# Optimization experiments

Measured on AMD Instinct MI355X. Metric: run time of the kernel, lower is better.

Reference implementation:

```python
import jax, jax.numpy as jnp
import numpy as np

IN_C, HID, LSTM_H, OUT_C = 128, 128, 128, 2
N_NODES, N_EDGES, N_GRAPHS = 100000, 1600000, 256


def gcn_conv(x, src, dst, W, b, n_nodes):
    # h = XW, then symmetric-normalized aggregation with self loops (PyG GCNConv defaults)
    h = x @ W  # [N, H]
    loop = jnp.arange(n_nodes)
    s = jnp.concatenate([src, loop])
    d = jnp.concatenate([dst, loop])
    deg = jax.ops.segment_sum(jnp.ones_like(d, dtype=h.dtype), d, num_segments=n_nodes)
    dinv = jnp.where(deg > 0, jax.lax.rsqrt(deg), 0.0)
    norm = dinv[s] * dinv[d]  # [E+N]
    out = jax.ops.segment_sum(norm[:, None] * h[s], d, num_segments=n_nodes)
    return out + b


def setup_inputs() -> dict:
    key = jax.random.key(0)
    ks = jax.random.split(key, 16)
    x = jax.random.normal(ks[0], (N_NODES, IN_C), dtype=jnp.float32)
    edge_index = jax.random.randint(ks[1], (2, N_EDGES), 0, N_NODES)
    batch = jnp.sort(jax.random.randint(ks[2], (N_NODES,), 0, N_GRAPHS))
    sc = lambda *shape: 1.0 / np.sqrt(shape[0])
    W0 = jax.random.normal(ks[3], (IN_C, HID), jnp.float32) * sc(IN_C)
    b0 = jnp.zeros((HID,), jnp.float32)
    W1 = jax.random.normal(ks[4], (HID, HID), jnp.float32) * sc(HID)
    b1 = jnp.zeros((HID,), jnp.float32)
    W2 = jax.random.normal(ks[5], (HID, HID), jnp.float32) * sc(HID)
    b2 = jnp.zeros((HID,), jnp.float32)
    W_ih = jax.random.normal(ks[6], (4 * LSTM_H, HID), jnp.float32) * sc(HID)
    W_hh = jax.random.normal(ks[7], (4 * LSTM_H, LSTM_H), jnp.float32) * sc(LSTM_H)
    b_ih = jnp.zeros((4 * LSTM_H,), jnp.float32)
    b_hh = jnp.zeros((4 * LSTM_H,), jnp.float32)
    W_fc = jax.random.normal(ks[8], (OUT_C, LSTM_H), jnp.float32) * sc(LSTM_H)
    b_fc = jnp.zeros((OUT_C,), jnp.float32)
    return dict(x=x, edge_index=edge_index, batch=batch, num_graphs=N_GRAPHS,
                W0=W0, b0=b0, W1=W1, b1=b1, W2=W2, b2=b2,
                W_ih=W_ih, W_hh=W_hh, b_ih=b_ih, b_hh=b_hh, W_fc=W_fc, b_fc=b_fc)


def reference(x, edge_index, batch, num_graphs, W0, b0, W1, b1, W2, b2,
              W_ih, W_hh, b_ih, b_hh, W_fc, b_fc):
    n_nodes = x.shape[0]
    src, dst = edge_index[0], edge_index[1]
    h = x
    for W, b in ((W0, b0), (W1, b1), (W2, b2)):
        h = jax.nn.relu(gcn_conv(h, src, dst, W, b, n_nodes))
    # dropout: identity in eval mode
    # global_mean_pool over batch ids
    sums = jax.ops.segment_sum(h, batch, num_segments=num_graphs)  # [G, HID]
    cnts = jax.ops.segment_sum(jnp.ones((n_nodes,), h.dtype), batch, num_segments=num_graphs)
    pooled = sums / jnp.maximum(cnts, 1.0)[:, None]
    # single-step LSTM from zero state: h0 = c0 = 0 => W_hh contributes 0
    g = pooled @ W_ih.T + b_ih + b_hh  # [G, 4H]
    i, f, gg, o = jnp.split(g, 4, axis=-1)  # PyTorch gate order i,f,g,o
    c = jax.nn.sigmoid(i) * jnp.tanh(gg)
    hn = jax.nn.sigmoid(o) * jnp.tanh(c)
    return hn @ W_fc.T + b_fc
```

## Files before the change

### kernel.cpp

```cpp
#include <hip/hip_runtime.h>
#include <math.h>
#include <stdint.h>

#define HID 128
#define SCAN_CHUNK 1024
#define NBUCK_MAX 512
#define EDGE_TILE 8192
#define GEMM_ROWS 128
#define XS_STRIDE 136

typedef short bf16x8 __attribute__((ext_vector_type(8)));
typedef float f32x4 __attribute__((ext_vector_type(4)));

__device__ __forceinline__ unsigned int f2bf(float f) {
    union { float f; uint32_t i; } u; u.f = f;
    uint32_t r = u.i + 0x7fffu + ((u.i >> 16) & 1u);
    return r >> 16;
}
__device__ __forceinline__ float bf2f_lo(uint32_t x) {
    union { uint32_t i; float f; } t; t.i = x << 16; return t.f;
}
__device__ __forceinline__ float bf2f_hi(uint32_t x) {
    union { uint32_t i; float f; } t; t.i = x & 0xffff0000u; return t.f;
}

__global__ __launch_bounds__(256) void scan_phase1(const int* __restrict__ cnt,
                                                   int* __restrict__ blockSums,
                                                   float* __restrict__ dinv, int nN) {
    __shared__ int sdata[256];
    const int t = threadIdx.x;
    const int idx = blockIdx.x * SCAN_CHUNK + t * 4;
    int v0 = 0, v1 = 0, v2 = 0, v3 = 0;
    if (idx + 3 < nN) {
        int4 v = *(const int4*)(cnt + idx);
        v0 = v.x; v1 = v.y; v2 = v.z; v3 = v.w;
        float4 dv;
        dv.x = rsqrtf((float)v0 + 1.0f);
        dv.y = rsqrtf((float)v1 + 1.0f);
        dv.z = rsqrtf((float)v2 + 1.0f);
        dv.w = rsqrtf((float)v3 + 1.0f);
        *(float4*)(dinv + idx) = dv;
    } else {
        if (idx     < nN) { v0 = cnt[idx];     dinv[idx]     = rsqrtf((float)v0 + 1.0f); }
        if (idx + 1 < nN) { v1 = cnt[idx + 1]; dinv[idx + 1] = rsqrtf((float)v1 + 1.0f); }
        if (idx + 2 < nN) { v2 = cnt[idx + 2]; dinv[idx + 2] = rsqrtf((float)v2 + 1.0f); }
        if (idx + 3 < nN) { v3 = cnt[idx + 3]; dinv[idx + 3] = rsqrtf((float)v3 + 1.0f); }
    }
    sdata[t] = v0 + v1 + v2 + v3;
    __syncthreads();
#pragma unroll
    for (int off = 128; off > 0; off >>= 1) {
        if (t < off) sdata[t] += sdata[t + off];
        __syncthreads();
    }
    if (t == 0) blockSums[blockIdx.x] = sdata[0];
}

__global__ __launch_bounds__(256) void scan_phase2(int* __restrict__ blockSums, int nB) {
    __shared__ int sd[256];
    const int t = threadIdx.x;
    sd[t] = (t < nB) ? blockSums[t] : 0;
    __syncthreads();
#pragma unroll
    for (int off = 1; off < 256; off <<= 1) {
        int v = sd[t];
        int add = (t >= off) ? sd[t - off] : 0;
        __syncthreads();
        sd[t] = v + add;
        __syncthreads();
    }
    if (t < nB) blockSums[t] = (t > 0) ? sd[t - 1] : 0;
}

__global__ __launch_bounds__(256) void scan_phase3(const int* __restrict__ cnt,
                                                   const int* __restrict__ blockOffsets,
                                                   int* __restrict__ rowptr, int nN, int nE) {
    __shared__ int sdata[256];
    const int t = threadIdx.x;
    const int idx = blockIdx.x * SCAN_CHUNK + t * 4;
    int v0 = 0, v1 = 0, v2 = 0, v3 = 0;
    if (idx + 3 < nN) {
        int4 v = *(const int4*)(cnt + idx);
        v0 = v.x; v1 = v.y; v2 = v.z; v3 = v.w;
    } else {
        if (idx     < nN) v0 = cnt[idx];
        if (idx + 1 < nN) v1 = cnt[idx + 1];
        if (idx + 2 < nN) v2 = cnt[idx + 2];
        if (idx + 3 < nN) v3 = cnt[idx + 3];
    }
    sdata[t] = v0 + v1 + v2 + v3;
    __syncthreads();
#pragma unroll
    for (int off = 1; off < 256; off <<= 1) {
        int v = sdata[t];
        int add = (t >= off) ? sdata[t - off] : 0;
        __syncthreads();
        sdata[t] = v + add;
        __syncthreads();
    }
    const int pre = blockOffsets[blockIdx.x] + ((t > 0) ? sdata[t - 1] : 0);
    if (idx + 3 < nN) {
        *(int4*)(rowptr + idx) = make_int4(pre, pre + v0, pre + v0 + v1, pre + v0 + v1 + v2);
    } else {
        if (idx     < nN) rowptr[idx]     = pre;
        if (idx + 1 < nN) rowptr[idx + 1] = pre + v0;
        if (idx + 2 < nN) rowptr[idx + 2] = pre + v0 + v1;
        if (idx + 3 < nN) rowptr[idx + 3] = pre + v0 + v1 + v2;
    }
    if (blockIdx.x == 0 && t == 0) rowptr[nN] = nE;
}

__global__ __launch_bounds__(256) void bucket_count(const int* __restrict__ dst,
                                                    int* __restrict__ bcnt, int nE, int nB) {
    __shared__ int h[NBUCK_MAX];
    for (int i = threadIdx.x; i < nB; i += 256) h[i] = 0;
    __syncthreads();
    const int base = blockIdx.x * EDGE_TILE;
    const int end = min(base + EDGE_TILE, nE);
    for (int e = base + threadIdx.x; e < end; e += 256)
        atomicAdd(&h[dst[e] >> 8], 1);
    __syncthreads();
    for (int i = threadIdx.x; i < nB; i += 256)
        if (h[i]) atomicAdd(&bcnt[i], h[i]);
}

__global__ __launch_bounds__(512) void bucket_scan(const int* __restrict__ bcnt,
                                                   int* __restrict__ boff,
                                                   int* __restrict__ bcur, int nB) {
    __shared__ int sd[512];
    const int t = threadIdx.x;
    sd[t] = (t < nB) ? bcnt[t] : 0;
    __syncthreads();
#pragma unroll
    for (int off = 1; off < 512; off <<= 1) {
        int v = sd[t];
        int add = (t >= off) ? sd[t - off] : 0;
        __syncthreads();
        sd[t] = v + add;
        __syncthreads();
    }
    if (t < nB) {
        int ex = (t > 0) ? sd[t - 1] : 0;
        boff[t] = ex;
        bcur[t] = ex;
    }
}

__global__ __launch_bounds__(256) void bucket_scatter(const int* __restrict__ src,
                                                      const int* __restrict__ dst,
                                                      int* __restrict__ bcur,
                                                      unsigned int* __restrict__ ebuf,
                                                      int nE, int nB) {
    __shared__ int h[NBUCK_MAX];
    __shared__ int basearr[NBUCK_MAX];
    const int base = blockIdx.x * EDGE_TILE;
    const int end = min(base + EDGE_TILE, nE);
    for (int i = threadIdx.x; i < nB; i += 256) h[i] = 0;
    __syncthreads();
    for (int e = base + threadIdx.x; e < end; e += 256)
        atomicAdd(&h[dst[e] >> 8], 1);
    __syncthreads();
    for (int i = threadIdx.x; i < nB; i += 256) {
        int c = h[i];
        basearr[i] = c ? atomicAdd(&bcur[i], c) : 0;
        h[i] = 0;
    }
    __syncthreads();
    for (int e = base + threadIdx.x; e < end; e += 256) {
        int d = dst[e];
        int b = d >> 8;
        int pos = basearr[b] + atomicAdd(&h[b], 1);
        ebuf[pos] = ((unsigned)src[e] << 8) | ((unsigned)d & 255u);
    }
}

__global__ __launch_bounds__(256) void node_count(const unsigned int* __restrict__ ebuf,
                                                  const int* __restrict__ boff,
                                                  int* __restrict__ cnt, int nE, int nB, int nN) {
    __shared__ int h[256];
    h[threadIdx.x] = 0;
    __syncthreads();
    const int b = blockIdx.x;
    const int e0 = boff[b];
    const int e1 = (b + 1 < nB) ? boff[b + 1] : nE;
    for (int e = e0 + threadIdx.x; e < e1; e += 256)
        atomicAdd(&h[ebuf[e] & 255u], 1);
    __syncthreads();
    const int v = b * 256 + threadIdx.x;
    if (v < nN) cnt[v] = h[threadIdx.x];
}

__global__ __launch_bounds__(256) void csr_from_buckets(const unsigned int* __restrict__ ebuf,
                                                        const int* __restrict__ boff,
                                                        const int* __restrict__ rowptr,
                                                        int* __restrict__ ssrc, int nE, int nB) {
    __shared__ int cur[256];
    const int b = blockIdx.x;
    const int e0 = boff[b];
    const int e1 = (b + 1 < nB) ? boff[b + 1] : nE;
    const int nodeBase = b * 256;
    cur[threadIdx.x] = 0;
    __syncthreads();
    for (int e = e0 + threadIdx.x; e < e1; e += 256) {
        unsigned int ed = ebuf[e];
        int li = (int)(ed & 255u);
        int pos = rowptr[nodeBase + li] + atomicAdd(&cur[li], 1);
        ssrc[pos] = (int)(ed >> 8);
    }
}

__global__ __launch_bounds__(256) void wt_kernel(const float* __restrict__ W0,
                                                 const float* __restrict__ W1,
                                                 const float* __restrict__ W2,
                                                 unsigned short* __restrict__ Wtb) {
    int i = blockIdx.x * 256 + threadIdx.x;
    if (i < 3 * HID * HID) {
        int w = i >> 14, r = i & 16383;
        int n = r >> 7, k = r & 127;
        const float* W = (w == 0) ? W0 : (w == 1) ? W1 : W2;
        Wtb[i] = (unsigned short)f2bf(W[k * HID + n]);
    }
}

__global__ __launch_bounds__(256) void gemm_mfma_f32in(const float* __restrict__ X,
                                                       const uint4* __restrict__ Wtb,
                                                       const float* __restrict__ dinv,
                                                       unsigned int* __restrict__ Pb32,
                                                       int nN) {
    __shared__ short Xs[GEMM_ROWS * XS_STRIDE];
    __shared__ short Ws[HID * XS_STRIDE];
    const int tid = threadIdx.x;
    const int rowBase = blockIdx.x * GEMM_ROWS;
#pragma unroll
    for (int it = 0; it < 16; ++it) {
        int f = it * 256 + tid;
        int row = f >> 5, c = f & 31;
        int grow = rowBase + row;
        float4 v = make_float4(0.f, 0.f, 0.f, 0.f);
        if (grow < nN) v = *(const float4*)(X + (size_t)grow * HID + c * 4);
        uint2 o;
        o.x = f2bf(v.x) | (f2bf(v.y) << 16);
        o.y = f2bf(v.z) | (f2bf(v.w) << 16);
        *(uint2*)(&Xs[row * XS_STRIDE + c * 4]) = o;
    }
#pragma unroll
    for (int it = 0; it < 8; ++it) {
        int f = it * 256 + tid;
        int n = f >> 4, c = f & 15;
        *(uint4*)(&Ws[n * XS_STRIDE + c * 8]) = Wtb[f];
    }
    __syncthreads();
    const int wave = tid >> 6, lane = tid & 63;
    const int quad = lane >> 4, l16 = lane & 15;
    f32x4 acc[2][8] = {};
    const int kq = quad * 8;
#pragma unroll
    for (int ks = 0; ks < 4; ++ks) {
        const int k0 = ks * 32 + kq;
        bf16x8 a0 = *(const bf16x8*)(&Xs[(wave * 32 + l16) * XS_STRIDE + k0]);
        bf16x8 a1 = *(const bf16x8*)(&Xs[(wave * 32 + 16 + l16) * XS_STRIDE + k0]);
#pragma unroll
        for (int nt = 0; nt < 8; ++nt) {
            bf16x8 b = *(const bf16x8*)(&Ws[(nt * 16 + l16) * XS_STRIDE + k0]);
            acc[0][nt] = __builtin_amdgcn_mfma_f32_16x16x32_bf16(a0, b, acc[0][nt], 0, 0, 0);
            acc[1][nt] = __builtin_amdgcn_mfma_f32_16x16x32_bf16(a1, b, acc[1][nt], 0, 0, 0);
        }
    }
#pragma unroll
    for (int mt = 0; mt < 2; ++mt) {
        const int gr0 = rowBase + wave * 32 + mt * 16 + quad * 4;
#pragma unroll
        for (int r = 0; r < 4; ++r) {
            const int gr = gr0 + r;
            const bool ok = gr < nN;
            const float d = ok ? dinv[gr] : 0.f;
#pragma unroll
            for (int nt = 0; nt < 8; ++nt) {
                float v = d * acc[mt][nt][r];
                float vo = __shfl_xor(v, 1, 64);
                if (ok && !(l16 & 1)) {
                    Pb32[(size_t)gr * 64 + nt * 8 + (l16 >> 1)] = f2bf(v) | (f2bf(vo) << 16);
                }
            }
        }
    }
}

__device__ __forceinline__ void acc_bf8(const uint4 q, float* a) {
    union { uint32_t i; float f; } t;
    t.i = q.x << 16;          a[0] += t.f;
    t.i = q.x & 0xffff0000u;  a[1] += t.f;
    t.i = q.y << 16;          a[2] += t.f;
    t.i = q.y & 0xffff0000u;  a[3] += t.f;
    t.i = q.z << 16;          a[4] += t.f;
    t.i = q.z & 0xffff0000u;  a[5] += t.f;
    t.i = q.w << 16;          a[6] += t.f;
    t.i = q.w & 0xffff0000u;  a[7] += t.f;
}

__global__ __launch_bounds__(256) void fused_agg_gemm(const uint4* __restrict__ Pb,
                                                      const int* __restrict__ rowptr,
                                                      const int* __restrict__ ssrc,
                                                      const float* __restrict__ dinv,
                                                      const float* __restrict__ bias,
                                                      const uint4* __restrict__ Wtb,
                                                      unsigned int* __restrict__ Pout32,
                                                      int nN) {
    __shared__ short Ws[HID * XS_STRIDE];
    __shared__ short Hs[16 * XS_STRIDE];
    const int tid = threadIdx.x;
#pragma unroll
    for (int it = 0; it < 8; ++it) {
        int f = it * 256 + tid;
        int n = f >> 4, c = f & 15;
        *(uint4*)(&Ws[n * XS_STRIDE + c * 8]) = Wtb[f];
    }
    const int lane16 = tid & 15;
    const int grp = tid >> 4;
    const int v = blockIdx.x * 16 + grp;
    const bool ok = v < nN;
    float a0[8], a1[8], a2[8], a3[8];
#pragma unroll
    for (int i = 0; i < 8; ++i) { a0[i] = 0.f; a1[i] = 0.f; a2[i] = 0.f; a3[i] = 0.f; }
    uint4 q = make_uint4(0u, 0u, 0u, 0u);
    if (ok) {
        acc_bf8(Pb[(size_t)v * 16 + lane16], a0);
        int e = rowptr[v];
        const int e1 = rowptr[v + 1];
        for (; e + 4 <= e1; e += 4) {
            const int u0 = ssrc[e + 0], u1 = ssrc[e + 1], u2 = ssrc[e + 2], u3 = ssrc[e + 3];
            uint4 q0 = Pb[(size_t)u0 * 16 + lane16];
            uint4 q1 = Pb[(size_t)u1 * 16 + lane16];
            uint4 q2 = Pb[(size_t)u2 * 16 + lane16];
            uint4 q3 = Pb[(size_t)u3 * 16 + lane16];
            acc_bf8(q0, a0); acc_bf8(q1, a1); acc_bf8(q2, a2); acc_bf8(q3, a3);
        }
        for (; e < e1; ++e) {
            uint4 qe = Pb[(size_t)ssrc[e] * 16 + lane16];
            acc_bf8(qe, a1);
        }
        const float dv = dinv[v];
        const float4 bb0 = ((const float4*)bias)[lane16 * 2];
        const float4 bb1 = ((const float4*)bias)[lane16 * 2 + 1];
        float4 o0, o1;
        o0.x = fmaxf(fmaf(dv, (a0[0] + a1[0]) + (a2[0] + a3[0]), bb0.x), 0.f);
        o0.y = fmaxf(fmaf(dv, (a0[1] + a1[1]) + (a2[1] + a3[1]), bb0.y), 0.f);
        o0.z = fmaxf(fmaf(dv, (a0[2] + a1[2]) + (a2[2] + a3[2]), bb0.z), 0.f);
        o0.w = fmaxf(fmaf(dv, (a0[3] + a1[3]) + (a2[3] + a3[3]), bb0.w), 0.f);
        o1.x = fmaxf(fmaf(dv, (a0[4] + a1[4]) + (a2[4] + a3[4]), bb1.x), 0.f);
        o1.y = fmaxf(fmaf(dv, (a0[5] + a1[5]) + (a2[5] + a3[5]), bb1.y), 0.f);
        o1.z = fmaxf(fmaf(dv, (a0[6] + a1[6]) + (a2[6] + a3[6]), bb1.z), 0.f);
        o1.w = fmaxf(fmaf(dv, (a0[7] + a1[7]) + (a2[7] + a3[7]), bb1.w), 0.f);
        q.x = f2bf(o0.x) | (f2bf(o0.y) << 16);
        q.y = f2bf(o0.z) | (f2bf(o0.w) << 16);
        q.z = f2bf(o1.x) | (f2bf(o1.y) << 16);
        q.w = f2bf(o1.z) | (f2bf(o1.w) << 16);
    }
    *(uint4*)(&Hs[grp * XS_STRIDE + lane16 * 8]) = q;
    __syncthreads();
    const int wave = tid >> 6, lane = tid & 63;
    const int quad = lane >> 4, l16 = lane & 15;
    f32x4 acc[2] = {};
#pragma unroll
    for (int ks = 0; ks < 4; ++ks) {
        const int k0 = ks * 32 + quad * 8;
        bf16x8 a = *(const bf16x8*)(&Hs[l16 * XS_STRIDE + k0]);
#pragma unroll
        for (int nt = 0; nt < 2; ++nt) {
            bf16x8 b = *(const bf16x8*)(&Ws[((wave * 2 + nt) * 16 + l16) * XS_STRIDE + k0]);
            acc[nt] = __builtin_amdgcn_mfma_f32_16x16x32_bf16(a, b, acc[nt], 0, 0, 0);
        }
    }
#pragma unroll
    for (int r = 0; r < 4; ++r) {
        const int gr = blockIdx.x * 16 + quad * 4 + r;
        const bool okr = gr < nN;
        const float d = okr ? dinv[gr] : 0.f;
#pragma unroll
        for (int nt = 0; nt < 2; ++nt) {
            float val = d * acc[nt][r];
            float vo = __shfl_xor(val, 1, 64);
            if (okr && !(l16 & 1)) {
                Pout32[(size_t)gr * 64 + (wave * 2 + nt) * 8 + (l16 >> 1)] =
                    f2bf(val) | (f2bf(vo) << 16);
            }
        }
    }
}

__global__ __launch_bounds__(256) void agg_kernel(const uint4* __restrict__ Pb,
                                                  const int* __restrict__ rowptr,
                                                  const int* __restrict__ ssrc,
                                                  const float* __restrict__ dinv,
                                                  const float* __restrict__ bias,
                                                  uint4* __restrict__ Xb_out, int nN) {
    const int lane = threadIdx.x & 15;
    const int grp = threadIdx.x >> 4;
    const int v = blockIdx.x * 16 + grp;
    if (v >= nN) return;
    float a0[8], a1[8], a2[8], a3[8];
#pragma unroll
    for (int i = 0; i < 8; ++i) { a0[i] = 0.f; a1[i] = 0.f; a2[i] = 0.f; a3[i] = 0.f; }
    acc_bf8(Pb[(size_t)v * 16 + lane], a0);
    int e = rowptr[v];
    const int e1 = rowptr[v + 1];
    for (; e + 4 <= e1; e += 4) {
        const int u0 = ssrc[e + 0], u1 = ssrc[e + 1], u2 = ssrc[e + 2], u3 = ssrc[e + 3];
        uint4 q0 = Pb[(size_t)u0 * 16 + lane];
        uint4 q1 = Pb[(size_t)u1 * 16 + lane];
        uint4 q2 = Pb[(size_t)u2 * 16 + lane];
        uint4 q3 = Pb[(size_t)u3 * 16 + lane];
        acc_bf8(q0, a0); acc_bf8(q1, a1); acc_bf8(q2, a2); acc_bf8(q3, a3);
    }
    for (; e < e1; ++e) {
        uint4 q = Pb[(size_t)ssrc[e] * 16 + lane];
        acc_bf8(q, a1);
    }
    const float dv = dinv[v];
    const float4 bb0 = ((const float4*)bias)[lane * 2];
    const float4 bb1 = ((const float4*)bias)[lane * 2 + 1];
    float4 o0, o1;
    o0.x = fmaxf(fmaf(dv, (a0[0] + a1[0]) + (a2[0] + a3[0]), bb0.x), 0.f);
    o0.y = fmaxf(fmaf(dv, (a0[1] + a1[1]) + (a2[1] + a3[1]), bb0.y), 0.f);
    o0.z = fmaxf(fmaf(dv, (a0[2] + a1[2]) + (a2[2] + a3[2]), bb0.z), 0.f);
    o0.w = fmaxf(fmaf(dv, (a0[3] + a1[3]) + (a2[3] + a3[3]), bb0.w), 0.f);
    o1.x = fmaxf(fmaf(dv, (a0[4] + a1[4]) + (a2[4] + a3[4]), bb1.x), 0.f);
    o1.y = fmaxf(fmaf(dv, (a0[5] + a1[5]) + (a2[5] + a3[5]), bb1.y), 0.f);
    o1.z = fmaxf(fmaf(dv, (a0[6] + a1[6]) + (a2[6] + a3[6]), bb1.z), 0.f);
    o1.w = fmaxf(fmaf(dv, (a0[7] + a1[7]) + (a2[7] + a3[7]), bb1.w), 0.f);
    uint4 q;
    q.x = f2bf(o0.x) | (f2bf(o0.y) << 16);
    q.y = f2bf(o0.z) | (f2bf(o0.w) << 16);
    q.z = f2bf(o1.x) | (f2bf(o1.y) << 16);
    q.w = f2bf(o1.z) | (f2bf(o1.w) << 16);
    Xb_out[(size_t)v * 16 + lane] = q;
}

__global__ __launch_bounds__(256) void pool_lstm(const unsigned int* __restrict__ Xb32,
                                                 const int* __restrict__ batch,
                                                 const float* __restrict__ W_ih,
                                                 const float* __restrict__ b_ih,
                                                 const float* __restrict__ b_hh,
                                                 const float* __restrict__ W_fc,
                                                 const float* __restrict__ b_fc,
                                                 float* __restrict__ out, int nN) {
    __shared__ float sred[4][HID];
    __shared__ float pv[HID];
    __shared__ float r0[4], r1[4];
    __shared__ int sbounds[2];
    const int g = blockIdx.x;
    const int tid = threadIdx.x;
    if (tid == 0) {
        int lo = 0, hi = nN;
        while (lo < hi) { int m = (lo + hi) >> 1; if (batch[m] < g) lo = m + 1; else hi = m; }
        sbounds[0] = lo;
        hi = nN;
        while (lo < hi) { int m = (lo + hi) >> 1; if (batch[m] < g + 1) lo = m + 1; else hi = m; }
        sbounds[1] = lo;
    }
    __syncthreads();
    const int s = sbounds[0], e = sbounds[1];
    const int c2 = tid & 63;
    const int st = tid >> 6;
    float acc0 = 0.f, acc1 = 0.f;
    int v = s + st;
    for (; v + 12 < e; v += 16) {
        unsigned int q0 = Xb32[(size_t)(v     ) * 64 + c2];
        unsigned int q1 = Xb32[(size_t)(v +  4) * 64 + c2];
        unsigned int q2 = Xb32[(size_t)(v +  8) * 64 + c2];
        unsigned int q3 = Xb32[(size_t)(v + 12) * 64 + c2];
        acc0 += (bf2f_lo(q0) + bf2f_lo(q1)) + (bf2f_lo(q2) + bf2f_lo(q3));
        acc1 += (bf2f_hi(q0) + bf2f_hi(q1)) + (bf2f_hi(q2) + bf2f_hi(q3));
    }
    for (; v < e; v += 4) {
        unsigned int q = Xb32[(size_t)v * 64 + c2];
        acc0 += bf2f_lo(q);
        acc1 += bf2f_hi(q);
    }
    sred[st][c2 * 2] = acc0;
    sred[st][c2 * 2 + 1] = acc1;
    __syncthreads();
    if (st == 0) {
        const float inv = 1.0f / (float)max(e - s, 1);
        pv[c2 * 2]     = ((sred[0][c2 * 2] + sred[1][c2 * 2]) +
                          (sred[2][c2 * 2] + sred[3][c2 * 2])) * inv;
        pv[c2 * 2 + 1] = ((sred[0][c2 * 2 + 1] + sred[1][c2 * 2 + 1]) +
                          (sred[2][c2 * 2 + 1] + sred[3][c2 * 2 + 1])) * inv;
    }
    __syncthreads();
    float p0 = 0.f, p1 = 0.f;
    if (tid < HID) {
        const int j = tid;
        float di = b_ih[j] + b_hh[j];
        float dg = b_ih[256 + j] + b_hh[256 + j];
        float dO = b_ih[384 + j] + b_hh[384 + j];
        const float4* pv4 = (const float4*)pv;
#pragma unroll 4
        for (int k4 = 0; k4 < 32; ++k4) {
            float4 p = pv4[k4];
            float4 wi = *(const float4*)(W_ih + (size_t)j * HID + k4 * 4);
            float4 wg = *(const float4*)(W_ih + (size_t)(256 + j) * HID + k4 * 4);
            float4 wo = *(const float4*)(W_ih + (size_t)(384 + j) * HID + k4 * 4);
            di += p.x * wi.x + p.y * wi.y + p.z * wi.z + p.w * wi.w;
            dg += p.x * wg.x + p.y * wg.y + p.z * wg.z + p.w * wg.w;
            dO += p.x * wo.x + p.y * wo.y + p.z * wo.z + p.w * wo.w;
        }
        const float si = 1.0f / (1.0f + expf(-di));
        const float so = 1.0f / (1.0f + expf(-dO));
        const float c = si * tanhf(dg);
        const float hn = so * tanhf(c);
        p0 = hn * W_fc[j];
        p1 = hn * W_fc[HID + j];
    }
#pragma unroll
    for (int off = 32; off > 0; off >>= 1) {
        p0 += __shfl_down(p0, off, 64);
        p1 += __shfl_down(p1, off, 64);
    }
    const int w = tid >> 6, l = tid & 63;
    if (l == 0) { r0[w] = p0; r1[w] = p1; }
    __syncthreads();
    if (tid == 0) {
        out[g * 2 + 0] = (r0[0] + r0[1]) + (r0[2] + r0[3]) + b_fc[0];
        out[g * 2 + 1] = (r1[0] + r1[1]) + (r1[2] + r1[3]) + b_fc[1];
    }
}

extern "C" void kernel_launch(void* const* d_in, const int* in_sizes, int n_in,
                              void* d_out, int out_size, void* d_ws, size_t ws_size,
                              hipStream_t stream) {
    const float* x      = (const float*)d_in[0];
    const int*   eidx   = (const int*)d_in[1];
    const int*   batch  = (const int*)d_in[2];
    const float* W0     = (const float*)d_in[4];
    const float* b0     = (const float*)d_in[5];
    const float* W1     = (const float*)d_in[6];
    const float* b1     = (const float*)d_in[7];
    const float* W2     = (const float*)d_in[8];
    const float* b2     = (const float*)d_in[9];
    const float* W_ih   = (const float*)d_in[10];
    const float* b_ih   = (const float*)d_in[12];
    const float* b_hh   = (const float*)d_in[13];
    const float* W_fc   = (const float*)d_in[14];
    const float* b_fc   = (const float*)d_in[15];
    float* out = (float*)d_out;

    const int nN = in_sizes[0] / HID;
    const int nE = in_sizes[1] / 2;
    const int nG = out_size / 2;
    const int* src = eidx;
    const int* dst = eidx + nE;
    const int rowsPad = (nN + GEMM_ROWS - 1) & ~(GEMM_ROWS - 1);

    size_t off = 0;
    auto alloc = [&](size_t bytes) -> void* {
        void* p = (char*)d_ws + off;
        off += (bytes + 255) & ~(size_t)255;
        return p;
    };
    uint4* Pb     = (uint4*)alloc((size_t)nN * 16 * sizeof(uint4));
    uint4* Pb2    = (uint4*)alloc((size_t)nN * 16 * sizeof(uint4));
    uint4* Xb     = (uint4*)alloc((size_t)nN * 16 * sizeof(uint4));
    float* dinv   = (float*)alloc((size_t)nN * sizeof(float));
    int*   cnt    = (int*)alloc((size_t)nN * sizeof(int));
    int*   rowptr = (int*)alloc((size_t)(nN + 1) * sizeof(int));
    int*   ssrc   = (int*)alloc((size_t)nE * sizeof(int));
    unsigned int* ebuf = (unsigned int*)alloc((size_t)nE * sizeof(unsigned int));
    int*   blockSums = (int*)alloc(1024 * sizeof(int));
    int*   bcnt   = (int*)alloc(NBUCK_MAX * sizeof(int));
    int*   boff   = (int*)alloc(NBUCK_MAX * sizeof(int));
    int*   bcur   = (int*)alloc(NBUCK_MAX * sizeof(int));
    unsigned short* Wtb = (unsigned short*)alloc(3 * HID * HID * sizeof(unsigned short));
    (void)ws_size;

    const int scanBlocks = (nN + SCAN_CHUNK - 1) / SCAN_CHUNK;
    const int nB = (nN + 255) >> 8;
    const int tileBlocks = (nE + EDGE_TILE - 1) / EDGE_TILE;

    hipMemsetAsync(bcnt, 0, NBUCK_MAX * sizeof(int), stream);
    bucket_count<<<tileBlocks, 256, 0, stream>>>(dst, bcnt, nE, nB);
    bucket_scan<<<1, 512, 0, stream>>>(bcnt, boff, bcur, nB);
    bucket_scatter<<<tileBlocks, 256, 0, stream>>>(src, dst, bcur, ebuf, nE, nB);

    node_count<<<nB, 256, 0, stream>>>(ebuf, boff, cnt, nE, nB, nN);
    scan_phase1<<<scanBlocks, 256, 0, stream>>>(cnt, blockSums, dinv, nN);
    scan_phase2<<<1, 256, 0, stream>>>(blockSums, scanBlocks);
    scan_phase3<<<scanBlocks, 256, 0, stream>>>(cnt, blockSums, rowptr, nN, nE);
    csr_from_buckets<<<nB, 256, 0, stream>>>(ebuf, boff, rowptr, ssrc, nE, nB);

    wt_kernel<<<(3 * HID * HID + 255) / 256, 256, 0, stream>>>(W0, W1, W2, Wtb);

    const int gemmBlocks = rowsPad / GEMM_ROWS;
    const int aggBlocks = (nN + 15) / 16;
    const uint4* Wt1 = (const uint4*)(Wtb + HID * HID);
    const uint4* Wt2 = (const uint4*)(Wtb + 2 * HID * HID);

    gemm_mfma_f32in<<<gemmBlocks, 256, 0, stream>>>(x, (const uint4*)Wtb, dinv,
                                                    (unsigned int*)Pb, nN);
    fused_agg_gemm<<<aggBlocks, 256, 0, stream>>>(Pb, rowptr, ssrc, dinv, b0, Wt1,
                                                  (unsigned int*)Pb2, nN);
    fused_agg_gemm<<<aggBlocks, 256, 0, stream>>>(Pb2, rowptr, ssrc, dinv, b1, Wt2,
                                                  (unsigned int*)Pb, nN);
    agg_kernel<<<aggBlocks, 256, 0, stream>>>(Pb, rowptr, ssrc, dinv, b2, Xb, nN);

    pool_lstm<<<nG, 256, 0, stream>>>((const unsigned int*)Xb, batch,
                                      W_ih, b_ih, b_hh, W_fc, b_fc, out, nN);
}
```

Measured before the change: 457.0 us.

## Build CSR in one cooperative kernel with global atomics and grid syncs

```diff
diff --git a/kernel.cpp b/kernel.cpp
--- a/kernel.cpp
+++ b/kernel.cpp
@@ -1,13 +1,12 @@
 #include <hip/hip_runtime.h>
+#include <hip/hip_cooperative_groups.h>
 #include <math.h>
 #include <stdint.h>
 
 #define HID 128
-#define SCAN_CHUNK 1024
-#define NBUCK_MAX 512
-#define EDGE_TILE 8192
 #define GEMM_ROWS 128
 #define XS_STRIDE 136
+#define NBLK 256
 
 typedef short bf16x8 __attribute__((ext_vector_type(8)));
 typedef float f32x4 __attribute__((ext_vector_type(4)));
@@ -24,201 +23,101 @@
     union { uint32_t i; float f; } t; t.i = x & 0xffff0000u; return t.f;
 }
 
-__global__ __launch_bounds__(256) void scan_phase1(const int* __restrict__ cnt,
-                                                   int* __restrict__ blockSums,
-                                                   float* __restrict__ dinv, int nN) {
-    __shared__ int sdata[256];
-    const int t = threadIdx.x;
-    const int idx = blockIdx.x * SCAN_CHUNK + t * 4;
-    int v0 = 0, v1 = 0, v2 = 0, v3 = 0;
-    if (idx + 3 < nN) {
-        int4 v = *(const int4*)(cnt + idx);
-        v0 = v.x; v1 = v.y; v2 = v.z; v3 = v.w;
-        float4 dv;
-        dv.x = rsqrtf((float)v0 + 1.0f);
-        dv.y = rsqrtf((float)v1 + 1.0f);
-        dv.z = rsqrtf((float)v2 + 1.0f);
-        dv.w = rsqrtf((float)v3 + 1.0f);
-        *(float4*)(dinv + idx) = dv;
-    } else {
-        if (idx     < nN) { v0 = cnt[idx];     dinv[idx]     = rsqrtf((float)v0 + 1.0f); }
-        if (idx + 1 < nN) { v1 = cnt[idx + 1]; dinv[idx + 1] = rsqrtf((float)v1 + 1.0f); }
-        if (idx + 2 < nN) { v2 = cnt[idx + 2]; dinv[idx + 2] = rsqrtf((float)v2 + 1.0f); }
-        if (idx + 3 < nN) { v3 = cnt[idx + 3]; dinv[idx + 3] = rsqrtf((float)v3 + 1.0f); }
-    }
-    sdata[t] = v0 + v1 + v2 + v3;
-    __syncthreads();
-#pragma unroll
-    for (int off = 128; off > 0; off >>= 1) {
-        if (t < off) sdata[t] += sdata[t + off];
-        __syncthreads();
-    }
-    if (t == 0) blockSums[blockIdx.x] = sdata[0];
-}
-
-__global__ __launch_bounds__(256) void scan_phase2(int* __restrict__ blockSums, int nB) {
+__global__ __launch_bounds__(256) void prep_coop(const int* __restrict__ src,
+                                                 const int* __restrict__ dst,
+                                                 const float* __restrict__ W0,
+                                                 const float* __restrict__ W1,
+                                                 const float* __restrict__ W2,
+                                                 int* __restrict__ cnt,
+                                                 float* __restrict__ dinv,
+                                                 int* __restrict__ rowptr,
+                                                 int* __restrict__ cur,
+                                                 int* __restrict__ ssrc,
+                                                 unsigned short* __restrict__ Wtb,
+                                                 int* __restrict__ blockSums,
+                                                 int nN, int nE) {
+    namespace cg = cooperative_groups;
+    cg::grid_group grid = cg::this_grid();
     __shared__ int sd[256];
     const int t = threadIdx.x;
-    sd[t] = (t < nB) ? blockSums[t] : 0;
-    __syncthreads();
-#pragma unroll
-    for (int off = 1; off < 256; off <<= 1) {
-        int v = sd[t];
-        int add = (t >= off) ? sd[t - off] : 0;
-        __syncthreads();
-        sd[t] = v + add;
-        __syncthreads();
-    }
-    if (t < nB) blockSums[t] = (t > 0) ? sd[t - 1] : 0;
-}
-
-__global__ __launch_bounds__(256) void scan_phase3(const int* __restrict__ cnt,
-                                                   const int* __restrict__ blockOffsets,
-                                                   int* __restrict__ rowptr, int nN, int nE) {
-    __shared__ int sdata[256];
-    const int t = threadIdx.x;
-    const int idx = blockIdx.x * SCAN_CHUNK + t * 4;
-    int v0 = 0, v1 = 0, v2 = 0, v3 = 0;
-    if (idx + 3 < nN) {
-        int4 v = *(const int4*)(cnt + idx);
-        v0 = v.x; v1 = v.y; v2 = v.z; v3 = v.w;
-    } else {
-        if (idx     < nN) v0 = cnt[idx];
-        if (idx + 1 < nN) v1 = cnt[idx + 1];
-        if (idx + 2 < nN) v2 = cnt[idx + 2];
-        if (idx + 3 < nN) v3 = cnt[idx + 3];
-    }
-    sdata[t] = v0 + v1 + v2 + v3;
-    __syncthreads();
-#pragma unroll
-    for (int off = 1; off < 256; off <<= 1) {
-        int v = sdata[t];
-        int add = (t >= off) ? sdata[t - off] : 0;
-        __syncthreads();
-        sdata[t] = v + add;
-        __syncthreads();
-    }
-    const int pre = blockOffsets[blockIdx.x] + ((t > 0) ? sdata[t - 1] : 0);
-    if (idx + 3 < nN) {
-        *(int4*)(rowptr + idx) = make_int4(pre, pre + v0, pre + v0 + v1, pre + v0 + v1 + v2);
-    } else {
-        if (idx     < nN) rowptr[idx]     = pre;
-        if (idx + 1 < nN) rowptr[idx + 1] = pre + v0;
-        if (idx + 2 < nN) rowptr[idx + 2] = pre + v0 + v1;
-        if (idx + 3 < nN) rowptr[idx + 3] = pre + v0 + v1 + v2;
-    }
-    if (blockIdx.x == 0 && t == 0) rowptr[nN] = nE;
-}
-
-__global__ __launch_bounds__(256) void bucket_count(const int* __restrict__ dst,
-                                                    int* __restrict__ bcnt, int nE, int nB) {
-    __shared__ int h[NBUCK_MAX];
-    for (int i = threadIdx.x; i < nB; i += 256) h[i] = 0;
-    __syncthreads();
-    const int base = blockIdx.x * EDGE_TILE;
-    const int end = min(base + EDGE_TILE, nE);
-    for (int e = base + threadIdx.x; e < end; e += 256)
-        atomicAdd(&h[dst[e] >> 8], 1);
-    __syncthreads();
-    for (int i = threadIdx.x; i < nB; i += 256)
-        if (h[i]) atomicAdd(&bcnt[i], h[i]);
-}
-
-__global__ __launch_bounds__(512) void bucket_scan(const int* __restrict__ bcnt,
-                                                   int* __restrict__ boff,
-                                                   int* __restrict__ bcur, int nB) {
-    __shared__ int sd[512];
-    const int t = threadIdx.x;
-    sd[t] = (t < nB) ? bcnt[t] : 0;
-    __syncthreads();
-#pragma unroll
-    for (int off = 1; off < 512; off <<= 1) {
-        int v = sd[t];
-        int add = (t >= off) ? sd[t - off] : 0;
-        __syncthreads();
-        sd[t] = v + add;
-        __syncthreads();
-    }
-    if (t < nB) {
-        int ex = (t > 0) ? sd[t - 1] : 0;
-        boff[t] = ex;
-        bcur[t] = ex;
-    }
-}
-
-__global__ __launch_bounds__(256) void bucket_scatter(const int* __restrict__ src,
-                                                      const int* __restrict__ dst,
-                                                      int* __restrict__ bcur,
-                                                      unsigned int* __restrict__ ebuf,
-                                                      int nE, int nB) {
-    __shared__ int h[NBUCK_MAX];
-    __shared__ int basearr[NBUCK_MAX];
-    const int base = blockIdx.x * EDGE_TILE;
-    const int end = min(base + EDGE_TILE, nE);
-    for (int i = threadIdx.x; i < nB; i += 256) h[i] = 0;
-    __syncthreads();
-    for (int e = base + threadIdx.x; e < end; e += 256)
-        atomicAdd(&h[dst[e] >> 8], 1);
-    __syncthreads();
-    for (int i = threadIdx.x; i < nB; i += 256) {
-        int c = h[i];
-        basearr[i] = c ? atomicAdd(&bcur[i], c) : 0;
-        h[i] = 0;
-    }
-    __syncthreads();
-    for (int e = base + threadIdx.x; e < end; e += 256) {
-        int d = dst[e];
-        int b = d >> 8;
-        int pos = basearr[b] + atomicAdd(&h[b], 1);
-        ebuf[pos] = ((unsigned)src[e] << 8) | ((unsigned)d & 255u);
-    }
-}
-
-__global__ __launch_bounds__(256) void node_count(const unsigned int* __restrict__ ebuf,
-                                                  const int* __restrict__ boff,
-                                                  int* __restrict__ cnt, int nE, int nB, int nN) {
-    __shared__ int h[256];
-    h[threadIdx.x] = 0;
-    __syncthreads();
     const int b = blockIdx.x;
-    const int e0 = boff[b];
-    const int e1 = (b + 1 < nB) ? boff[b + 1] : nE;
-    for (int e = e0 + threadIdx.x; e < e1; e += 256)
-        atomicAdd(&h[ebuf[e] & 255u], 1);
-    __syncthreads();
-    const int v = b * 256 + threadIdx.x;
-    if (v < nN) cnt[v] = h[threadIdx.x];
-}
-
-__global__ __launch_bounds__(256) void csr_from_buckets(const unsigned int* __restrict__ ebuf,
-                                                        const int* __restrict__ boff,
-                                                        const int* __restrict__ rowptr,
-                                                        int* __restrict__ ssrc, int nE, int nB) {
-    __shared__ int cur[256];
-    const int b = blockIdx.x;
-    const int e0 = boff[b];
-    const int e1 = (b + 1 < nB) ? boff[b + 1] : nE;
-    const int nodeBase = b * 256;
-    cur[threadIdx.x] = 0;
-    __syncthreads();
-    for (int e = e0 + threadIdx.x; e < e1; e += 256) {
-        unsigned int ed = ebuf[e];
-        int li = (int)(ed & 255u);
-        int pos = rowptr[nodeBase + li] + atomicAdd(&cur[li], 1);
-        ssrc[pos] = (int)(ed >> 8);
-    }
-}
-
-__global__ __launch_bounds__(256) void wt_kernel(const float* __restrict__ W0,
-                                                 const float* __restrict__ W1,
-                                                 const float* __restrict__ W2,
-                                                 unsigned short* __restrict__ Wtb) {
-    int i = blockIdx.x * 256 + threadIdx.x;
-    if (i < 3 * HID * HID) {
+    const int gtid = b * 256 + t;
+    const int gsz = NBLK * 256;
+    const int CH = (((nN + NBLK - 1) / NBLK) + 1) & ~1;
+    const int base = b * CH;
+
+    for (int i = gtid; i < 3 * HID * HID; i += gsz) {
         int w = i >> 14, r = i & 16383;
         int n = r >> 7, k = r & 127;
         const float* W = (w == 0) ? W0 : (w == 1) ? W1 : W2;
         Wtb[i] = (unsigned short)f2bf(W[k * HID + n]);
+    }
+    for (int e = gtid; e < nE; e += gsz)
+        atomicAdd(&cnt[dst[e]], 1);
+    __threadfence();
+    grid.sync();
+
+    int ssum = 0;
+    for (int k = t; k < CH; k += 256) {
+        int i = base + k;
+        if (i < nN) ssum += cnt[i];
+    }
+    sd[t] = ssum;
+    __syncthreads();
+#pragma unroll
+    for (int off = 128; off > 0; off >>= 1) {
+        if (t < off) sd[t] += sd[t + off];
+        __syncthreads();
+    }
+    if (t == 0) blockSums[b] = sd[0];
+    __threadfence();
+    grid.sync();
+
+    if (b == 0) {
+        int v = blockSums[t];
+        sd[t] = v;
+        __syncthreads();
+#pragma unroll
+        for (int off = 1; off < 256; off <<= 1) {
+            int vv = sd[t];
+            int add = (t >= off) ? sd[t - off] : 0;
+            __syncthreads();
+            sd[t] = vv + add;
+            __syncthreads();
+        }
+        blockSums[t] = sd[t] - v;
+    }
+    __threadfence();
+    grid.sync();
+
+    const int bOff = blockSums[b];
+    const int i0 = base + 2 * t, i1 = i0 + 1;
+    const bool k0 = (2 * t < CH) && (i0 < nN);
+    const bool k1 = (2 * t + 1 < CH) && (i1 < nN);
+    const int a0v = k0 ? cnt[i0] : 0;
+    const int a1v = k1 ? cnt[i1] : 0;
+    const int s = a0v + a1v;
+    sd[t] = s;
+    __syncthreads();
+#pragma unroll
+    for (int off = 1; off < 256; off <<= 1) {
+        int vv = sd[t];
+        int add = (t >= off) ? sd[t - off] : 0;
+        __syncthreads();
+        sd[t] = vv + add;
+        __syncthreads();
+    }
+    const int o0 = bOff + (sd[t] - s);
+    if (k0) { rowptr[i0] = o0;       cur[i0] = o0;       dinv[i0] = rsqrtf((float)a0v + 1.0f); }
+    if (k1) { rowptr[i1] = o0 + a0v; cur[i1] = o0 + a0v; dinv[i1] = rsqrtf((float)a1v + 1.0f); }
+    if (b == NBLK - 1 && t == 0) rowptr[nN] = nE;
+    __threadfence();
+    grid.sync();
+
+    for (int e = gtid; e < nE; e += gsz) {
+        const int d = dst[e];
+        const int pos = atomicAdd(&cur[d], 1);
+        ssrc[pos] = src[e];
     }
 }
 
@@ -545,8 +444,8 @@
     const float* b_fc   = (const float*)d_in[15];
     float* out = (float*)d_out;
 
-    const int nN = in_sizes[0] / HID;
-    const int nE = in_sizes[1] / 2;
+    int nN = in_sizes[0] / HID;
+    int nE = in_sizes[1] / 2;
     const int nG = out_size / 2;
     const int* src = eidx;
     const int* dst = eidx + nE;
@@ -563,32 +462,20 @@
     uint4* Xb     = (uint4*)alloc((size_t)nN * 16 * sizeof(uint4));
     float* dinv   = (float*)alloc((size_t)nN * sizeof(float));
     int*   cnt    = (int*)alloc((size_t)nN * sizeof(int));
+    int*   cur    = (int*)alloc((size_t)nN * sizeof(int));
     int*   rowptr = (int*)alloc((size_t)(nN + 1) * sizeof(int));
     int*   ssrc   = (int*)alloc((size_t)nE * sizeof(int));
-    unsigned int* ebuf = (unsigned int*)alloc((size_t)nE * sizeof(unsigned int));
-    int*   blockSums = (int*)alloc(1024 * sizeof(int));
-    int*   bcnt   = (int*)alloc(NBUCK_MAX * sizeof(int));
-    int*   boff   = (int*)alloc(NBUCK_MAX * sizeof(int));
-    int*   bcur   = (int*)alloc(NBUCK_MAX * sizeof(int));
+    int*   blockSums = (int*)alloc(NBLK * sizeof(int));
     unsigned short* Wtb = (unsigned short*)alloc(3 * HID * HID * sizeof(unsigned short));
     (void)ws_size;
 
-    const int scanBlocks = (nN + SCAN_CHUNK - 1) / SCAN_CHUNK;
-    const int nB = (nN + 255) >> 8;
-    const int tileBlocks = (nE + EDGE_TILE - 1) / EDGE_TILE;
-
-    hipMemsetAsync(bcnt, 0, NBUCK_MAX * sizeof(int), stream);
-    bucket_count<<<tileBlocks, 256, 0, stream>>>(dst, bcnt, nE, nB);
-    bucket_scan<<<1, 512, 0, stream>>>(bcnt, boff, bcur, nB);
-    bucket_scatter<<<tileBlocks, 256, 0, stream>>>(src, dst, bcur, ebuf, nE, nB);
-
-    node_count<<<nB, 256, 0, stream>>>(ebuf, boff, cnt, nE, nB, nN);
-    scan_phase1<<<scanBlocks, 256, 0, stream>>>(cnt, blockSums, dinv, nN);
-    scan_phase2<<<1, 256, 0, stream>>>(blockSums, scanBlocks);
-    scan_phase3<<<scanBlocks, 256, 0, stream>>>(cnt, blockSums, rowptr, nN, nE);
-    csr_from_buckets<<<nB, 256, 0, stream>>>(ebuf, boff, rowptr, ssrc, nE, nB);
-
-    wt_kernel<<<(3 * HID * HID + 255) / 256, 256, 0, stream>>>(W0, W1, W2, Wtb);
+    hipMemsetAsync(cnt, 0, (size_t)nN * sizeof(int), stream);
+    void* pargs[] = { (void*)&src, (void*)&dst, (void*)&W0, (void*)&W1, (void*)&W2,
+                      (void*)&cnt, (void*)&dinv, (void*)&rowptr, (void*)&cur,
+                      (void*)&ssrc, (void*)&Wtb, (void*)&blockSums,
+                      (void*)&nN, (void*)&nE };
+    hipLaunchCooperativeKernel((const void*)prep_coop, dim3(NBLK), dim3(256),
+                               pargs, 0, stream);
 
     const int gemmBlocks = rowsPad / GEMM_ROWS;
     const int aggBlocks = (nN + 15) / 16;
```

New measurement: 771.1 us. 1.69x slower.
